# Kernel optimization log

Measured on AMD Instinct MI355X. Metric: run time of the kernel, lower is better.

## Reference

```python
import jax, jax.numpy as jnp
import numpy as np

B, T, D, H = 8, 2048, 512, 128

def setup_inputs() -> dict:
    key = jax.random.key(0)
    ks = jax.random.split(key, 8)
    s = lambda fan_in: 1.0 / np.sqrt(fan_in)
    return {
        "x": jax.random.normal(ks[0], (B, T, D), jnp.float32),
        "prediction": jax.random.normal(ks[1], (B, T, D), jnp.float32),
        "Wq": jax.random.uniform(ks[2], (D, H), jnp.float32, -s(D), s(D)),
        "bq": jnp.zeros((H,), jnp.float32),
        "Wk": jax.random.uniform(ks[3], (D, H), jnp.float32, -s(D), s(D)),
        "bk": jnp.zeros((H,), jnp.float32),
        "Wv": jax.random.uniform(ks[4], (D, D), jnp.float32, -s(D), s(D)),
        "bv": jnp.zeros((D,), jnp.float32),
        "Wf": jax.random.uniform(ks[5], (2 * D, D), jnp.float32, -s(2 * D), s(2 * D)),
        "bf": jnp.zeros((D,), jnp.float32),
    }

def reference(x, prediction, Wq, bq, Wk, bk, Wv, bv, Wf, bf):
    # q,k: [B,T,H]; v: [B,T,D]
    q = jnp.einsum('btd,dh->bth', prediction, Wq) + bq
    k = jnp.einsum('btd,dh->bth', x, Wk) + bk
    v = jnp.einsum('btd,de->bte', x, Wv) + bv
    # unscaled attention scores [B,T,T]
    scores = jnp.einsum('bth,bsh->bts', q, k)
    attn = jax.nn.softmax(scores, axis=-1)
    attended = jnp.einsum('bts,bsd->btd', attn, v)
    fusion_input = jnp.concatenate([prediction, attended], axis=-1)  # [B,T,2D]
    return jax.nn.sigmoid(jnp.einsum('btf,fd->btd', fusion_input, Wf) + bf)
```

## Files before the change

### kernel.cpp

```cpp
#include <hip/hip_runtime.h>
#include <hip/hip_bf16.h>


#define APF_B 8
#define APF_T 2048
#define APF_D 512
#define APF_H 128
#define APF_M (APF_B * APF_T)
#define FA_SB 128

typedef unsigned short u16;
typedef __attribute__((ext_vector_type(8))) short short8;
typedef __attribute__((ext_vector_type(4))) float f32x4;
typedef __attribute__((ext_vector_type(16))) float f32x16;

static __device__ __forceinline__ u16 f2bf(float x) {
    union { float f; unsigned int u; } cv;
    cv.f = x;
    unsigned int u = cv.u + 0x7FFFu + ((cv.u >> 16) & 1u);
    return (u16)(u >> 16);
}

static __device__ __forceinline__ void load16_lds(const u16* g, u16* l) {
    __builtin_amdgcn_global_load_lds(
        (const __attribute__((address_space(1))) unsigned int*)g,
        (__attribute__((address_space(3))) unsigned int*)l,
        16, 0, 0);
}

static __device__ __forceinline__ f32x16 zero16() {
    f32x16 v;
#pragma unroll
    for (int i = 0; i < 16; ++i) v[i] = 0.f;
    return v;
}


__global__ __launch_bounds__(256) void prep_w(
    const float* __restrict__ Wq, u16* __restrict__ WqT,
    const float* __restrict__ Wk, u16* __restrict__ WkT,
    const float* __restrict__ Wv, u16* __restrict__ WvT,
    const float* __restrict__ Wf, u16* __restrict__ WfT)
{
    const long e = blockIdx.x * 256L + threadIdx.x;
    if (e < 65536) {
        const long idx = e;
        const long n = idx / 512, k = idx % 512;
        WqT[idx] = f2bf(Wq[k * 128 + n]);
    } else if (e < 131072) {
        const long idx = e - 65536;
        const long n = idx / 512, k = idx % 512;
        WkT[idx] = f2bf(Wk[k * 128 + n]);
    } else if (e < 393216) {
        const long idx = e - 131072;
        const long n = idx / 512, k = idx % 512;
        WvT[idx] = f2bf(Wv[k * 512 + n]);
    } else if (e < 917504) {
        const long idx = e - 393216;
        const long n = idx / 1024, k = idx % 1024;
        WfT[idx] = f2bf(Wf[k * 512 + n]);
    }
}

template <int ADT, int BDT, int EPI, int BIASM, int VBLK>
static __device__ __forceinline__ void gemm_body(
    u16 (&smA)[2][4096], u16 (&smB)[2][4096],
    const void* Ap, const void* A2p, long lda,
    const void* Bp, long ldb,
    const float* bias, void* Cp, long ldc, int K,
    long row0, long col0)
{
    const int tid  = threadIdx.x;
    const int lane = tid & 63;
    const int wid  = tid >> 6;
    const int wr   = wid >> 1;
    const int wc   = wid & 1;

    f32x4 acc[4][4];
#pragma unroll
    for (int i = 0; i < 4; ++i)
#pragma unroll
        for (int j = 0; j < 4; ++j)
            acc[i][j] = (f32x4){0.f, 0.f, 0.f, 0.f};

    const int lrow = (lane >> 4) * 4;
    const int lcol = lane & 15;
    const int q8   = (lane >> 4) * 8;

    float4 ra[2][2], rb[2][2];

    auto loadA = [&](int kb) {
        if (ADT == 1 || (ADT == 2 && kb < APF_D)) {
            const float* Af = (const float*)Ap;
#pragma unroll
            for (int rep = 0; rep < 2; ++rep) {
                const int c = tid + rep * 256;
                const int rr = c >> 2, kc = (c & 3) * 8;
                const float* ga = Af + (row0 + rr) * lda + kb + kc;
                ra[rep][0] = *(const float4*)ga;
                ra[rep][1] = *(const float4*)(ga + 4);
            }
        }
    };
    auto loadB = [&](int kb) {
        if (BDT == 1) {
            const float* Bf = (const float*)Bp;
#pragma unroll
            for (int rep = 0; rep < 2; ++rep) {
                const int c = tid + rep * 256;
                const int rr = c >> 2, kc = (c & 3) * 8;
                const float* gb = Bf + (col0 + rr) * ldb + kb + kc;
                rb[rep][0] = *(const float4*)gb;
                rb[rep][1] = *(const float4*)(gb + 4);
            }
        }
    };
    auto dmaA = [&](int buf, int kb) {
        if (ADT == 0 || (ADT == 2 && kb >= APF_D)) {
            const u16* Ab = (ADT == 2) ? (const u16*)A2p : (const u16*)Ap;
            const int kk = (ADT == 2) ? kb - APF_D : kb;
            const long ld = (ADT == 2) ? APF_D : lda;
#pragma unroll
            for (int rep = 0; rep < 2; ++rep) {
                const int c = tid + rep * 256;
                const int rr = c >> 2, kc = (c & 3) * 8;
                const int wbase = (wid * 64 + rep * 256) * 8;
                load16_lds(Ab + (row0 + rr) * ld + kk + kc, &smA[buf][wbase]);
            }
        }
    };
    auto dmaB = [&](int buf, int kb) {
        if (BDT == 0) {
            const u16* Bb = (const u16*)Bp;
#pragma unroll
            for (int rep = 0; rep < 2; ++rep) {
                const int c = tid + rep * 256;
                const int rr = c >> 2, kc = (c & 3) * 8;
                const int wbase = (wid * 64 + rep * 256) * 8;
                load16_lds(Bb + (col0 + rr) * ldb + kb + kc, &smB[buf][wbase]);
            }
        }
    };
    auto cvt8 = [&](const float4& a, const float4& b) {
        short8 v;
        v[0] = (short)f2bf(a.x); v[1] = (short)f2bf(a.y);
        v[2] = (short)f2bf(a.z); v[3] = (short)f2bf(a.w);
        v[4] = (short)f2bf(b.x); v[5] = (short)f2bf(b.y);
        v[6] = (short)f2bf(b.z); v[7] = (short)f2bf(b.w);
        return v;
    };
    auto writeA = [&](int buf, int kb) {
        if (ADT == 1 || (ADT == 2 && kb < APF_D)) {
#pragma unroll
            for (int rep = 0; rep < 2; ++rep) {
                const int c = tid + rep * 256;
                *(short8*)&smA[buf][c * 8] = cvt8(ra[rep][0], ra[rep][1]);
            }
        }
    };
    auto writeB = [&](int buf, int kb) {
        if (BDT == 1) {
#pragma unroll
            for (int rep = 0; rep < 2; ++rep) {
                const int c = tid + rep * 256;
                *(short8*)&smB[buf][c * 8] = cvt8(rb[rep][0], rb[rep][1]);
            }
        }
    };

    const int NT = K / 32;
    loadA(0); loadB(0);
    writeA(0, 0); writeB(0, 0);
    dmaA(0, 0); dmaB(0, 0);

    int cur = 0;
    for (int t = 0; t < NT; ++t) {
        const int kb2 = (t + 1) * 32;
        if (t + 1 < NT) { loadA(kb2); loadB(kb2); }
        __syncthreads();
        if (t + 1 < NT) { dmaA(cur ^ 1, kb2); dmaB(cur ^ 1, kb2); }

        short8 av[4], bv4[4];
#pragma unroll
        for (int ti = 0; ti < 4; ++ti)
            av[ti] = *(const short8*)&smA[cur][(wr * 64 + ti * 16 + lcol) * 32 + q8];
#pragma unroll
        for (int tj = 0; tj < 4; ++tj)
            bv4[tj] = *(const short8*)&smB[cur][(wc * 64 + tj * 16 + lcol) * 32 + q8];

#pragma unroll
        for (int ti = 0; ti < 4; ++ti)
#pragma unroll
            for (int tj = 0; tj < 4; ++tj)
                acc[ti][tj] = __builtin_amdgcn_mfma_f32_16x16x32_bf16(
                    av[ti], bv4[tj], acc[ti][tj], 0, 0, 0);

        if (t + 1 < NT) { writeA(cur ^ 1, kb2); writeB(cur ^ 1, kb2); }
        cur ^= 1;
    }

#pragma unroll
    for (int ti = 0; ti < 4; ++ti) {
        const long m0t = row0 + wr * 64 + ti * 16 + lrow;
#pragma unroll
        for (int tj = 0; tj < 4; ++tj) {
            const long n = col0 + wc * 64 + tj * 16 + lcol;
            const float bn = (BIASM == 0) ? bias[n] : 0.f;
            if (EPI == 0) {
                u16* C = (u16*)Cp;
#pragma unroll
                for (int r = 0; r < 4; ++r) {
                    const long m = m0t + r;
                    const float bm = (BIASM == 1) ? bias[m] : bn;
                    long idx;
                    if (VBLK) {
                        idx = ((((m >> 5) * 256) + (n >> 3)) << 8) +
                              ((m & 31) << 3) + (n & 7);
                    } else {
                        idx = m * ldc + n;
                    }
                    C[idx] = f2bf(acc[ti][tj][r] + bm);
                }
            } else {
                float* C = (float*)Cp;
#pragma unroll
                for (int r = 0; r < 4; ++r) {
                    const float val = acc[ti][tj][r] + bn;
                    C[(m0t + r) * ldc + n] = 1.0f / (1.0f + expf(-val));
                }
            }
        }
    }
}

__global__ __launch_bounds__(256, 3) void mid_gemms(
    const float* __restrict__ x, const float* __restrict__ pred,
    const u16* __restrict__ WqT, const u16* __restrict__ WkT,
    const u16* __restrict__ WvT,
    const float* __restrict__ bq, const float* __restrict__ bk,
    const float* __restrict__ bv,
    u16* __restrict__ qb, u16* __restrict__ kbuf, u16* __restrict__ vTb)
{
    __shared__ u16 smA[2][4096];
    __shared__ u16 smB[2][4096];

    const int bid = blockIdx.x;
    if (bid < 256) {
        const int zz = bid >> 7, by = bid & 127;
        gemm_body<1, 0, 0, 0, 0>(smA, smB,
            zz ? (const void*)x : (const void*)pred, nullptr, APF_D,
            zz ? WkT : WqT, APF_D,
            zz ? bk : bq, zz ? (void*)kbuf : (void*)qb, APF_H, APF_D,
            (long)by * 128, 0);
    } else {
        const int t = bid - 256;
        const int zz = t >> 6, rem = t & 63;
        const int bx = rem & 15, by = rem >> 4;
        gemm_body<0, 1, 0, 1, 1>(smA, smB,
            WvT, nullptr, APF_D,
            (const void*)(x + (long)zz * APF_T * APF_D), APF_D,
            bv, (void*)(vTb + (long)zz * 1048576L), APF_T, APF_D,
            (long)by * 128, (long)bx * 128);
    }
}

__global__ __launch_bounds__(256, 2) void fusion_gemm(
    const float* __restrict__ pred, const u16* __restrict__ attb,
    const u16* __restrict__ WfT, const float* __restrict__ bfu,
    float* __restrict__ out)
{
    __shared__ u16 smA[2][4096];
    __shared__ u16 smB[2][4096];
    gemm_body<2, 0, 2, 0, 0>(smA, smB,
        (const void*)pred, (const void*)attb, APF_D,
        WfT, 2 * APF_D,
        bfu, (void*)out, APF_D, 2 * APF_D,
        (long)blockIdx.y * 128, (long)blockIdx.x * 128);
}

__global__ __launch_bounds__(256, 3) void attn_fused(
    const u16* __restrict__ qg, const u16* __restrict__ kg,
    const u16* __restrict__ vTg, u16* __restrict__ attg)
{
    __shared__ u16 sQ[64 * 128];
    __shared__ u16 sK[64 * 128];
    __shared__ u16 sP[64 * 64];
    __shared__ float sRS[192];

    const int tid  = threadIdx.x;
    const int lane = tid & 63;
    const int w    = tid >> 6;
    const int l31  = lane & 31;
    const int hi   = lane >> 5;
    const int qb   = w >> 1;
    const int sb   = w & 1;

    const int  bid = blockIdx.x;
    const long z   = bid & 7;
    const int  r   = bid >> 3;
    const long q0  = (long)(r & 31) * 64;
    const long d0  = (long)(r >> 5) * 256;

    const u16* kbase0 = kg + z * (long)APF_T * APF_H;

    {
        const u16* qsrc = qg + (z * APF_T + q0) * APF_H;
#pragma unroll
        for (int rep = 0; rep < 4; ++rep) {
            const int c    = tid + rep * 256;
            const int row  = c >> 4;
            const int col8 = (c & 15) * 8;
            load16_lds(qsrc + row * APF_H + (col8 ^ ((row & 15) << 3)), &sQ[c * 8]);
        }
#pragma unroll
        for (int rep = 0; rep < 4; ++rep) {
            const int c    = tid + rep * 256;
            const int row  = c >> 4;
            const int col8 = (c & 15) * 8;
            load16_lds(kbase0 + row * APF_H + (col8 ^ ((row & 15) << 3)), &sK[c * 8]);
        }
    }
    __syncthreads();

    f32x16 oacc[2][2];
#pragma unroll
    for (int i = 0; i < 2; ++i)
#pragma unroll
        for (int j = 0; j < 2; ++j) oacc[i][j] = zero16();
    f32x16 rsacc = zero16();

    const long dblk0 = (d0 >> 5) + w * 2;
    const u16* vzb = vTg + z * 1048576L + dblk0 * 65536L + (long)l31 * 8;

    const int qrow = qb * 32 + l31;
    const int krow = sb * 32 + l31;
    const int pcol = sb * 32 + l31;

    for (int kt = 0; kt < APF_T / 64; ++kt) {
        f32x16 sacc = zero16();
#pragma unroll
        for (int ks = 0; ks < 8; ++ks) {
            const int colk = ks * 16 + hi * 8;
            const short8 av = *(const short8*)&sQ[qrow * 128 + (colk ^ ((qrow & 15) << 3))];
            const short8 bv = *(const short8*)&sK[krow * 128 + (colk ^ ((krow & 15) << 3))];
            sacc = __builtin_amdgcn_mfma_f32_32x32x16_bf16(av, bv, sacc, 0, 0, 0);
        }
        __syncthreads();

        if (kt + 1 < APF_T / 64) {
            const u16* ksrc = kbase0 + (long)(kt + 1) * 64 * APF_H;
#pragma unroll
            for (int rep = 0; rep < 4; ++rep) {
                const int c    = tid + rep * 256;
                const int row  = c >> 4;
                const int col8 = (c & 15) * 8;
                load16_lds(ksrc + row * APF_H + (col8 ^ ((row & 15) << 3)), &sK[c * 8]);
            }
        }

        const long sbase = (long)kt * 8 + hi;
        short8 vf1[2][2];
#pragma unroll
        for (int dt = 0; dt < 2; ++dt)
#pragma unroll
            for (int ks = 0; ks < 2; ++ks)
                vf1[dt][ks] = *(const short8*)(vzb + dt * 65536L + (sbase + ks * 2) * 256);

#pragma unroll
        for (int rg = 0; rg < 16; ++rg) {
            const float e = __expf(sacc[rg]);
            rsacc[rg] += e;
            const int prow = qb * 32 + (rg & 3) + 8 * (rg >> 2) + 4 * hi;
            sP[prow * 64 + (pcol ^ ((prow & 7) << 3))] = f2bf(e);
        }
        __syncthreads();

#pragma unroll
        for (int ks = 0; ks < 2; ++ks) {
            const int colk = ks * 16 + hi * 8;
            short8 pa[2];
#pragma unroll
            for (int qt = 0; qt < 2; ++qt) {
                const int prow = qt * 32 + l31;
                pa[qt] = *(const short8*)&sP[prow * 64 + (colk ^ ((prow & 7) << 3))];
            }
#pragma unroll
            for (int dt = 0; dt < 2; ++dt)
#pragma unroll
                for (int qt = 0; qt < 2; ++qt)
                    oacc[qt][dt] = __builtin_amdgcn_mfma_f32_32x32x16_bf16(
                        pa[qt], vf1[dt][ks], oacc[qt][dt], 0, 0, 0);
        }

        short8 vf2[2][2];
#pragma unroll
        for (int dt = 0; dt < 2; ++dt)
#pragma unroll
            for (int ks = 0; ks < 2; ++ks)
                vf2[dt][ks] = *(const short8*)(vzb + dt * 65536L + (sbase + (ks + 2) * 2) * 256);

#pragma unroll
        for (int ks = 0; ks < 2; ++ks) {
            const int colk = (ks + 2) * 16 + hi * 8;
            short8 pa[2];
#pragma unroll
            for (int qt = 0; qt < 2; ++qt) {
                const int prow = qt * 32 + l31;
                pa[qt] = *(const short8*)&sP[prow * 64 + (colk ^ ((prow & 7) << 3))];
            }
#pragma unroll
            for (int dt = 0; dt < 2; ++dt)
#pragma unroll
                for (int qt = 0; qt < 2; ++qt)
                    oacc[qt][dt] = __builtin_amdgcn_mfma_f32_32x32x16_bf16(
                        pa[qt], vf2[dt][ks], oacc[qt][dt], 0, 0, 0);
        }
    }

#pragma unroll
    for (int rg = 0; rg < 16; ++rg) {
        float s = rsacc[rg];
        s += __shfl_xor(s, 1);
        s += __shfl_xor(s, 2);
        s += __shfl_xor(s, 4);
        s += __shfl_xor(s, 8);
        s += __shfl_xor(s, 16);
        rsacc[rg] = s;
    }
    if (l31 == 0) {
#pragma unroll
        for (int rg = 0; rg < 16; ++rg) {
            const int row = (rg & 3) + 8 * (rg >> 2) + 4 * hi;
            sRS[w * 32 + row] = rsacc[rg];
        }
    }
    __syncthreads();
    if (tid < 64) {
        const int qb2 = tid >> 5, r2 = tid & 31;
        sRS[128 + tid] = 1.0f / (sRS[(qb2 * 2 + 0) * 32 + r2] +
                                 sRS[(qb2 * 2 + 1) * 32 + r2]);
    }
    __syncthreads();

    const long rowg0 = z * APF_T + q0;
    const long colg0 = d0 + (long)w * 64;
#pragma unroll
    for (int qt = 0; qt < 2; ++qt)
#pragma unroll
        for (int rg = 0; rg < 16; ++rg) {
            const int row = qt * 32 + (rg & 3) + 8 * (rg >> 2) + 4 * hi;
            const float inv = sRS[128 + row];
#pragma unroll
            for (int dt = 0; dt < 2; ++dt)
                attg[(rowg0 + row) * APF_D + colg0 + dt * 32 + l31] =
                    f2bf(oacc[qt][dt][rg] * inv);
        }
}

extern "C" void kernel_launch(void* const* d_in, const int* in_sizes, int n_in,
                              void* d_out, int out_size, void* d_ws, size_t ws_size,
                              hipStream_t stream)
{
    (void)in_sizes; (void)n_in; (void)out_size; (void)ws_size;

    const float* x    = (const float*)d_in[0];
    const float* pred = (const float*)d_in[1];
    const float* Wq   = (const float*)d_in[2];
    const float* bq   = (const float*)d_in[3];
    const float* Wk   = (const float*)d_in[4];
    const float* bk   = (const float*)d_in[5];
    const float* Wv   = (const float*)d_in[6];
    const float* bv   = (const float*)d_in[7];
    const float* Wf   = (const float*)d_in[8];
    const float* bfu  = (const float*)d_in[9];

    u16* wsp  = (u16*)d_ws;
    u16* qb   = wsp;
    u16* kbuf = qb   + (long)APF_M * APF_H;
    u16* vTb  = kbuf + (long)APF_M * APF_H;
    u16* attb = vTb  + (long)APF_M * APF_D;
    u16* WqT  = attb + (long)APF_M * APF_D;
    u16* WkT  = WqT  + (long)APF_H * APF_D;
    u16* WvT  = WkT  + (long)APF_H * APF_D;
    u16* WfT  = WvT  + (long)APF_D * APF_D;

    const dim3 thr(256);

    prep_w<<<dim3(3584), thr, 0, stream>>>(Wq, WqT, Wk, WkT, Wv, WvT, Wf, WfT);

    mid_gemms<<<dim3(768), thr, 0, stream>>>(
        x, pred, WqT, WkT, WvT, bq, bk, bv, qb, kbuf, vTb);

    attn_fused<<<dim3(512), thr, 0, stream>>>(qb, kbuf, vTb, attb);

    fusion_gemm<<<dim3(4, 128), thr, 0, stream>>>(pred, attb, WfT, bfu,
                                                  (float*)d_out);
}
```

Baseline: 254.0 us.

## Split fusion GEMM: precompute prediction half early, add attention half later

The prediction half of the fusion GEMM (pred @ Wf[:512]) now runs as extra blocks inside mid_gemms and writes an fp32 partial result to workspace. The final fusion_gemm then covers only K=512 over the attention output and adds the partial before the sigmoid, so the attention-dependent tail does half the work. The weight prep kernel becomes a tiled LDS transpose with coalesced loads and vector stores, and float-to-bf16 conversion uses the hardware intrinsic. In exchange, a 32 MB fp32 intermediate is written and read back, which adds memory traffic.

```diff
diff --git a/kernel.cpp b/kernel.cpp
--- a/kernel.cpp
+++ b/kernel.cpp
@@ -7,7 +7,6 @@
 #define APF_D 512
 #define APF_H 128
 #define APF_M (APF_B * APF_T)
-#define FA_SB 128
 
 typedef unsigned short u16;
 typedef __attribute__((ext_vector_type(8))) short short8;
@@ -20,6 +19,11 @@
     unsigned int u = cv.u + 0x7FFFu + ((cv.u >> 16) & 1u);
     return (u16)(u >> 16);
 }
+static __device__ __forceinline__ u16 f2bf_hw(float x) {
+    union { __hip_bfloat16 h; u16 u; } cv;
+    cv.h = __float2bfloat16(x);
+    return cv.u;
+}
 
 static __device__ __forceinline__ void load16_lds(const u16* g, u16* l) {
     __builtin_amdgcn_global_load_lds(
@@ -34,7 +38,6 @@
     for (int i = 0; i < 16; ++i) v[i] = 0.f;
     return v;
 }
-
 
 __global__ __launch_bounds__(256) void prep_w(
     const float* __restrict__ Wq, u16* __restrict__ WqT,
@@ -42,33 +45,45 @@
     const float* __restrict__ Wv, u16* __restrict__ WvT,
     const float* __restrict__ Wf, u16* __restrict__ WfT)
 {
-    const long e = blockIdx.x * 256L + threadIdx.x;
-    if (e < 65536) {
-        const long idx = e;
-        const long n = idx / 512, k = idx % 512;
-        WqT[idx] = f2bf(Wq[k * 128 + n]);
-    } else if (e < 131072) {
-        const long idx = e - 65536;
-        const long n = idx / 512, k = idx % 512;
-        WkT[idx] = f2bf(Wk[k * 128 + n]);
-    } else if (e < 393216) {
-        const long idx = e - 131072;
-        const long n = idx / 512, k = idx % 512;
-        WvT[idx] = f2bf(Wv[k * 512 + n]);
-    } else if (e < 917504) {
-        const long idx = e - 393216;
-        const long n = idx / 1024, k = idx % 1024;
-        WfT[idx] = f2bf(Wf[k * 512 + n]);
+    __shared__ float tile[64][65];
+    int b = blockIdx.x;
+    const float* src; u16* dst; int K, N;
+    if (b < 16)      { src = Wq; dst = WqT; K = 512;  N = 128; }
+    else if (b < 32) { b -= 16; src = Wk; dst = WkT; K = 512;  N = 128; }
+    else if (b < 96) { b -= 32; src = Wv; dst = WvT; K = 512;  N = 512; }
+    else             { b -= 96; src = Wf; dst = WfT; K = 1024; N = 512; }
+    const int ntN = N >> 6;
+    const int k0 = (b / ntN) * 64, n0 = (b % ntN) * 64;
+
+    const int tid = threadIdx.x;
+#pragma unroll
+    for (int rep = 0; rep < 4; ++rep) {
+        const int r = (tid >> 4) + rep * 16;
+        const int c = (tid & 15) * 4;
+        const float4 v = *(const float4*)&src[(long)(k0 + r) * N + n0 + c];
+        tile[r][c] = v.x; tile[r][c + 1] = v.y;
+        tile[r][c + 2] = v.z; tile[r][c + 3] = v.w;
+    }
+    __syncthreads();
+#pragma unroll
+    for (int rep = 0; rep < 2; ++rep) {
+        const int rn = (tid >> 3) + rep * 32;
+        const int ck = (tid & 7) * 8;
+        short8 o;
+#pragma unroll
+        for (int j = 0; j < 8; ++j)
+            o[j] = (short)f2bf_hw(tile[ck + j][rn]);
+        *(short8*)&dst[(long)(n0 + rn) * K + k0 + ck] = o;
     }
 }
 
 template <int ADT, int BDT, int EPI, int BIASM, int VBLK>
 static __device__ __forceinline__ void gemm_body(
     u16 (&smA)[2][4096], u16 (&smB)[2][4096],
-    const void* Ap, const void* A2p, long lda,
+    const void* Ap, long lda,
     const void* Bp, long ldb,
     const float* bias, void* Cp, long ldc, int K,
-    long row0, long col0)
+    long row0, long col0, const float* Cadd)
 {
     const int tid  = threadIdx.x;
     const int lane = tid & 63;
@@ -90,7 +105,7 @@
     float4 ra[2][2], rb[2][2];
 
     auto loadA = [&](int kb) {
-        if (ADT == 1 || (ADT == 2 && kb < APF_D)) {
+        if (ADT == 1) {
             const float* Af = (const float*)Ap;
 #pragma unroll
             for (int rep = 0; rep < 2; ++rep) {
@@ -116,16 +131,14 @@
         }
     };
     auto dmaA = [&](int buf, int kb) {
-        if (ADT == 0 || (ADT == 2 && kb >= APF_D)) {
-            const u16* Ab = (ADT == 2) ? (const u16*)A2p : (const u16*)Ap;
-            const int kk = (ADT == 2) ? kb - APF_D : kb;
-            const long ld = (ADT == 2) ? APF_D : lda;
+        if (ADT == 0) {
+            const u16* Ab = (const u16*)Ap;
 #pragma unroll
             for (int rep = 0; rep < 2; ++rep) {
                 const int c = tid + rep * 256;
                 const int rr = c >> 2, kc = (c & 3) * 8;
                 const int wbase = (wid * 64 + rep * 256) * 8;
-                load16_lds(Ab + (row0 + rr) * ld + kk + kc, &smA[buf][wbase]);
+                load16_lds(Ab + (row0 + rr) * lda + kb + kc, &smA[buf][wbase]);
             }
         }
     };
@@ -143,14 +156,14 @@
     };
     auto cvt8 = [&](const float4& a, const float4& b) {
         short8 v;
-        v[0] = (short)f2bf(a.x); v[1] = (short)f2bf(a.y);
-        v[2] = (short)f2bf(a.z); v[3] = (short)f2bf(a.w);
-        v[4] = (short)f2bf(b.x); v[5] = (short)f2bf(b.y);
-        v[6] = (short)f2bf(b.z); v[7] = (short)f2bf(b.w);
+        v[0] = (short)f2bf_hw(a.x); v[1] = (short)f2bf_hw(a.y);
+        v[2] = (short)f2bf_hw(a.z); v[3] = (short)f2bf_hw(a.w);
+        v[4] = (short)f2bf_hw(b.x); v[5] = (short)f2bf_hw(b.y);
+        v[6] = (short)f2bf_hw(b.z); v[7] = (short)f2bf_hw(b.w);
         return v;
     };
-    auto writeA = [&](int buf, int kb) {
-        if (ADT == 1 || (ADT == 2 && kb < APF_D)) {
+    auto writeA = [&](int buf) {
+        if (ADT == 1) {
 #pragma unroll
             for (int rep = 0; rep < 2; ++rep) {
                 const int c = tid + rep * 256;
@@ -158,7 +171,7 @@
             }
         }
     };
-    auto writeB = [&](int buf, int kb) {
+    auto writeB = [&](int buf) {
         if (BDT == 1) {
 #pragma unroll
             for (int rep = 0; rep < 2; ++rep) {
@@ -170,7 +183,7 @@
 
     const int NT = K / 32;
     loadA(0); loadB(0);
-    writeA(0, 0); writeB(0, 0);
+    writeA(0); writeB(0);
     dmaA(0, 0); dmaB(0, 0);
 
     int cur = 0;
@@ -195,7 +208,7 @@
                 acc[ti][tj] = __builtin_amdgcn_mfma_f32_16x16x32_bf16(
                     av[ti], bv4[tj], acc[ti][tj], 0, 0, 0);
 
-        if (t + 1 < NT) { writeA(cur ^ 1, kb2); writeB(cur ^ 1, kb2); }
+        if (t + 1 < NT) { writeA(cur ^ 1); writeB(cur ^ 1); }
         cur ^= 1;
     }
 
@@ -205,7 +218,7 @@
 #pragma unroll
         for (int tj = 0; tj < 4; ++tj) {
             const long n = col0 + wc * 64 + tj * 16 + lcol;
-            const float bn = (BIASM == 0) ? bias[n] : 0.f;
+            const float bn = (BIASM == 0 && bias != nullptr) ? bias[n] : 0.f;
             if (EPI == 0) {
                 u16* C = (u16*)Cp;
 #pragma unroll
@@ -221,13 +234,25 @@
                     }
                     C[idx] = f2bf(acc[ti][tj][r] + bm);
                 }
-            } else {
+            } else if (EPI == 2) {
                 float* C = (float*)Cp;
 #pragma unroll
                 for (int r = 0; r < 4; ++r) {
                     const float val = acc[ti][tj][r] + bn;
                     C[(m0t + r) * ldc + n] = 1.0f / (1.0f + expf(-val));
                 }
+            } else if (EPI == 3) {
+                float* C = (float*)Cp;
+#pragma unroll
+                for (int r = 0; r < 4; ++r)
+                    C[(m0t + r) * ldc + n] = acc[ti][tj][r] + bn;
+            } else {
+                float* C = (float*)Cp;
+#pragma unroll
+                for (int r = 0; r < 4; ++r) {
+                    const float val = acc[ti][tj][r] + Cadd[(m0t + r) * ldc + n];
+                    C[(m0t + r) * ldc + n] = 1.0f / (1.0f + expf(-val));
+                }
             }
         }
     }
@@ -236,10 +261,11 @@
 __global__ __launch_bounds__(256, 3) void mid_gemms(
     const float* __restrict__ x, const float* __restrict__ pred,
     const u16* __restrict__ WqT, const u16* __restrict__ WkT,
-    const u16* __restrict__ WvT,
+    const u16* __restrict__ WvT, const u16* __restrict__ WfT,
     const float* __restrict__ bq, const float* __restrict__ bk,
-    const float* __restrict__ bv,
-    u16* __restrict__ qb, u16* __restrict__ kbuf, u16* __restrict__ vTb)
+    const float* __restrict__ bv, const float* __restrict__ bfu,
+    u16* __restrict__ qb, u16* __restrict__ kbuf, u16* __restrict__ vTb,
+    float* __restrict__ Cpre)
 {
     __shared__ u16 smA[2][4096];
     __shared__ u16 smB[2][4096];
@@ -248,34 +274,41 @@
     if (bid < 256) {
         const int zz = bid >> 7, by = bid & 127;
         gemm_body<1, 0, 0, 0, 0>(smA, smB,
-            zz ? (const void*)x : (const void*)pred, nullptr, APF_D,
+            zz ? (const void*)x : (const void*)pred, APF_D,
             zz ? WkT : WqT, APF_D,
             zz ? bk : bq, zz ? (void*)kbuf : (void*)qb, APF_H, APF_D,
-            (long)by * 128, 0);
-    } else {
+            (long)by * 128, 0, nullptr);
+    } else if (bid < 768) {
         const int t = bid - 256;
         const int zz = t >> 6, rem = t & 63;
         const int bx = rem & 15, by = rem >> 4;
         gemm_body<0, 1, 0, 1, 1>(smA, smB,
-            WvT, nullptr, APF_D,
+            WvT, APF_D,
             (const void*)(x + (long)zz * APF_T * APF_D), APF_D,
             bv, (void*)(vTb + (long)zz * 1048576L), APF_T, APF_D,
-            (long)by * 128, (long)bx * 128);
+            (long)by * 128, (long)bx * 128, nullptr);
+    } else {
+        const int t = bid - 768;
+        const int bx = t & 3, by = t >> 2;
+        gemm_body<1, 0, 3, 0, 0>(smA, smB,
+            (const void*)pred, APF_D,
+            WfT, 1024,
+            bfu, (void*)Cpre, APF_D, APF_D,
+            (long)by * 128, (long)bx * 128, nullptr);
     }
 }
 
 __global__ __launch_bounds__(256, 2) void fusion_gemm(
-    const float* __restrict__ pred, const u16* __restrict__ attb,
-    const u16* __restrict__ WfT, const float* __restrict__ bfu,
-    float* __restrict__ out)
+    const u16* __restrict__ attb, const u16* __restrict__ WfT,
+    const float* __restrict__ Cpre, float* __restrict__ out)
 {
     __shared__ u16 smA[2][4096];
     __shared__ u16 smB[2][4096];
-    gemm_body<2, 0, 2, 0, 0>(smA, smB,
-        (const void*)pred, (const void*)attb, APF_D,
-        WfT, 2 * APF_D,
-        bfu, (void*)out, APF_D, 2 * APF_D,
-        (long)blockIdx.y * 128, (long)blockIdx.x * 128);
+    gemm_body<0, 0, 4, 0, 0>(smA, smB,
+        (const void*)attb, APF_D,
+        WfT + 512, 1024,
+        nullptr, (void*)out, APF_D, APF_D,
+        (long)blockIdx.y * 128, (long)blockIdx.x * 128, Cpre);
 }
 
 __global__ __launch_bounds__(256, 3) void attn_fused(
@@ -474,7 +507,8 @@
     const float* Wf   = (const float*)d_in[8];
     const float* bfu  = (const float*)d_in[9];
 
-    u16* wsp  = (u16*)d_ws;
+    float* Cpre = (float*)d_ws;
+    u16* wsp  = (u16*)(Cpre + (long)APF_M * APF_D);
     u16* qb   = wsp;
     u16* kbuf = qb   + (long)APF_M * APF_H;
     u16* vTb  = kbuf + (long)APF_M * APF_H;
@@ -486,13 +520,13 @@
 
     const dim3 thr(256);
 
-    prep_w<<<dim3(3584), thr, 0, stream>>>(Wq, WqT, Wk, WkT, Wv, WvT, Wf, WfT);
-
-    mid_gemms<<<dim3(768), thr, 0, stream>>>(
-        x, pred, WqT, WkT, WvT, bq, bk, bv, qb, kbuf, vTb);
+    prep_w<<<dim3(224), thr, 0, stream>>>(Wq, WqT, Wk, WkT, Wv, WvT, Wf, WfT);
+
+    mid_gemms<<<dim3(1280), thr, 0, stream>>>(
+        x, pred, WqT, WkT, WvT, WfT, bq, bk, bv, bfu, qb, kbuf, vTb, Cpre);
 
     attn_fused<<<dim3(512), thr, 0, stream>>>(qb, kbuf, vTb, attb);
 
-    fusion_gemm<<<dim3(4, 128), thr, 0, stream>>>(pred, attb, WfT, bfu,
+    fusion_gemm<<<dim3(4, 128), thr, 0, stream>>>(attb, WfT, Cpre,
                                                   (float*)d_out);
 }
```

New measurement: 254.3 us. No clear change (+0.1%).
